# Kernel optimization log

Measured on AMD Instinct MI355X. Metric: run time of the kernel, lower is better.

Reference implementation:

```python
import jax, jax.numpy as jnp
import numpy as np


def conv3d(x, w, b, pad):
    # x: (B,C,D,H,W), w: (O,I,kd,kh,kw)
    y = jax.lax.conv_general_dilated(
        x, w, window_strides=(1, 1, 1), padding=[(pad, pad)] * 3,
        dimension_numbers=('NCDHW', 'OIDHW', 'NCDHW'))
    return y + b[None, :, None, None, None]


def setup_inputs() -> dict:
    key = jax.random.key(0)
    ks = jax.random.split(key, 8)
    B, C, D, H, W = 8, 128, 16, 32, 32
    C8 = C // 8
    return {
        'x': jax.random.normal(ks[0], (B, C, D, H, W), dtype=jnp.float32),
        'gamma': jax.random.normal(ks[1], (1,), dtype=jnp.float32),
        'w_k': jax.random.normal(ks[2], (C8, C, 1, 1, 1), dtype=jnp.float32) * 0.05,
        'b_k': jax.random.normal(ks[3], (C8,), dtype=jnp.float32) * 0.05,
        'w_q': jax.random.normal(ks[4], (C8, C, 1, 1, 1), dtype=jnp.float32) * 0.05,
        'b_q': jax.random.normal(ks[5], (C8,), dtype=jnp.float32) * 0.05,
        'w_v': jax.random.normal(ks[6], (C, C, 3, 3, 3), dtype=jnp.float32) * 0.02,
        'b_v': jax.random.normal(ks[7], (C,), dtype=jnp.float32) * 0.05,
    }


def reference(x, gamma, w_k, b_k, w_q, b_q, w_v, b_v):
    B, C, D, H, W = x.shape
    HW = H * W
    k = conv3d(x, w_k, b_k, 0)   # (B, C/8, D, H, W)
    q = conv3d(x, w_q, b_q, 0)   # (B, C/8, D, H, W)
    v = conv3d(x, w_v, b_v, 1)   # (B, C, D, H, W)

    # --- spatial (P) attention over HW positions, feature dim (C/8)*D ---
    kf = k.reshape(B, -1, HW)
    qf = q.reshape(B, -1, HW)
    # cor[b,s,t] = sum_f k[b,f,s] q[b,f,t]; softmax over t
    A_p = jax.nn.softmax(jnp.einsum('bfs,bft->bst', kf, qf), axis=-1)  # (B,HW,HW)
    vf = v.reshape(B, C * D, HW)
    # Patt[b,m,j] = sum_t v[b,m,t] A_p[b,j,t]  (v @ A_p^T)
    Patt = jnp.einsum('bmt,bjt->bmj', vf, A_p).reshape(B, C, D, H, W)

    # --- depth (D) attention over D slices, feature dim (C/8)*H*W ---
    kd = k.transpose(0, 2, 1, 3, 4).reshape(B, D, -1)
    qd = q.transpose(0, 2, 1, 3, 4).reshape(B, D, -1)
    A_d = jax.nn.softmax(jnp.einsum('bdf,bef->bde', kd, qd), axis=-1)  # (B,D,D)
    vd = v.transpose(0, 2, 1, 3, 4).reshape(B, D, -1)  # (B, D, C*H*W)
    # Datt[b,j,f] = sum_d A_d[b,j,d] vd[b,d,f]
    Datt = jnp.einsum('bjd,bdf->bjf', A_d, vd).reshape(B, D, C, H, W)
    Datt = Datt.transpose(0, 2, 1, 3, 4)  # (B,C,D,H,W)

    return gamma[0] * (Patt + Datt) + x
```

## Files before the change

kernel.cpp:

```cpp
#include <hip/hip_runtime.h>

#define HW   1024
#define DHW  16384

typedef __attribute__((ext_vector_type(8))) short short8;
typedef __attribute__((ext_vector_type(4))) float f32x4;

static __device__ __forceinline__ ushort f2bf(float f) {
  unsigned u = __float_as_uint(f);
  unsigned r = (u + 0x7fffu + ((u >> 16) & 1u)) >> 16;
  return (ushort)r;
}
static __device__ __forceinline__ float bf2f(ushort u) {
  return __uint_as_float(((unsigned)u) << 16);
}
static __device__ __forceinline__ void async_copy16(const ushort* g, ushort* l) {
  __builtin_amdgcn_global_load_lds(
      (const __attribute__((address_space(1))) unsigned int*)g,
      (__attribute__((address_space(3))) unsigned int*)l, 16, 0, 0);
}

__global__ __launch_bounds__(256) void prep_kernel(
    const float* __restrict__ x, const float* __restrict__ wk,
    const float* __restrict__ bk, const float* __restrict__ wq,
    const float* __restrict__ bq, const float* __restrict__ wv,
    float* __restrict__ k, float* __restrict__ q,
    ushort* __restrict__ xt, ushort* __restrict__ wt,
    ushort* __restrict__ zbuf) {
  __shared__ float wks[2048];
  __shared__ float wqs[2048];
  int gid = blockIdx.x;
  int tid = threadIdx.x;
  if (gid >= 512) {
    if (gid == 512 && tid < 512) zbuf[tid] = 0;
    int i = (gid - 512) * 256 + tid;
    int c8 = i & 7;
    int t = i >> 3;
    int o = t & 127; t >>= 7;
    int tap = t % 9; t /= 9;
    int chunk = t & 15;
    int kd = t >> 4;
    wt[i] = f2bf(wv[(size_t)(o * 128 + chunk * 8 + c8) * 27 + kd * 9 + tap]);
    return;
  }
  for (int i = tid; i < 2048; i += 256) {
    int c = i >> 4, o = i & 15;
    wks[i] = wk[o * 128 + c];
    wqs[i] = wq[o * 128 + c];
  }
  __syncthreads();
  int b = gid >> 6, bx = gid & 63;
  int p = bx * 256 + tid;
  int z = p >> 10, hw = p & 1023;
  float ak[16], aq[16];
#pragma unroll
  for (int o = 0; o < 16; ++o) { ak[o] = 0.f; aq[o] = 0.f; }
  const float* xb = x + (size_t)b * 128 * DHW + p;
  ushort* xtp = xt + (((size_t)(b * 16 + z) * 16) * 1024 + hw) * 8;
  for (int chunk = 0; chunk < 16; ++chunk) {
    ushort pack[8];
#pragma unroll
    for (int c8 = 0; c8 < 8; ++c8) {
      int c = chunk * 8 + c8;
      float xv = xb[(size_t)c * DHW];
      pack[c8] = f2bf(xv);
      const float4* wkc = (const float4*)&wks[c * 16];
      const float4* wqc = (const float4*)&wqs[c * 16];
#pragma unroll
      for (int g = 0; g < 4; ++g) {
        float4 wa = wkc[g], wb = wqc[g];
        ak[g * 4 + 0] += wa.x * xv; ak[g * 4 + 1] += wa.y * xv;
        ak[g * 4 + 2] += wa.z * xv; ak[g * 4 + 3] += wa.w * xv;
        aq[g * 4 + 0] += wb.x * xv; aq[g * 4 + 1] += wb.y * xv;
        aq[g * 4 + 2] += wb.z * xv; aq[g * 4 + 3] += wb.w * xv;
      }
    }
    *(uint4*)&xtp[(size_t)chunk * 1024 * 8] = *(const uint4*)pack;
  }
#pragma unroll
  for (int o = 0; o < 16; ++o) {
    k[((size_t)b * 16 + o) * DHW + p] = ak[o] + bk[o];
    q[((size_t)b * 16 + o) * DHW + p] = aq[o] + bq[o];
  }
}

__global__ __launch_bounds__(256, 2) void vconv_mfma_kernel(
    const ushort* __restrict__ xt, const ushort* __restrict__ wt,
    const float* __restrict__ bv, const ushort* __restrict__ zbuf,
    ushort* __restrict__ v) {
  __shared__ __align__(16) ushort xs[1536 * 8];
  __shared__ __align__(16) ushort wsm[2304 * 8];
  int tid = threadIdx.x;
  int wave = tid >> 6;
  int ml = tid & 15;
  int quad = (tid >> 4) & 3;
  int bz = blockIdx.x;
  int b = bz & 7, z = bz >> 3;
  int h0 = blockIdx.y * 8;
  int o0 = blockIdx.z * 64;

  f32x4 acc[4][4];
#pragma unroll
  for (int s = 0; s < 4; ++s)
#pragma unroll
    for (int t = 0; t < 4; ++t) acc[s][t] = (f32x4){0.f, 0.f, 0.f, 0.f};

  int cb0[4];
#pragma unroll
  for (int t = 0; t < 4; ++t)
    cb0[t] = (wave * 2 + (t >> 1)) * 34 + (t & 1) * 16 + ml;

  int xoff[6]; bool okx[6];
#pragma unroll
  for (int it = 0; it < 6; ++it) {
    int i = it * 256 + tid;
    int cu = i / 340;
    int cell = i - cu * 340;
    int hr = cell / 34;
    int wc = cell - hr * 34;
    int h = h0 + hr - 1, ww = wc - 1;
    okx[it] = (i < 1360) && ((unsigned)h < 32u) && ((unsigned)ww < 32u);
    xoff[it] = cu * 1024 + h * 32 + ww;
  }
  int woff[9];
#pragma unroll
  for (int it = 0; it < 9; ++it) {
    int i = it * 256 + tid;
    int cu = i / 576;
    int r = i - cu * 576;
    int tap = r >> 6, ol = r & 63;
    woff[it] = (cu * 9 + tap) * 128 + o0 + ol;
  }

  const int KH[9] = {0, 0, 0, 1, 1, 1, 2, 2, 2};
  const int KW[9] = {0, 1, 2, 0, 1, 2, 0, 1, 2};

  for (int kd = 0; kd < 3; ++kd) {
    int zd = z + kd - 1;
    bool zok = (zd >= 0 && zd < 16);
    int zdc = zok ? zd : 0;
    const ushort* xbase = xt + (size_t)(b * 16 + zdc) * 16 * 1024 * 8;
    for (int cb = 0; cb < 4; ++cb) {
      const ushort* xsb = xbase + (size_t)cb * 4 * 1024 * 8;
      const ushort* wsb = wt + (size_t)(kd * 16 + cb * 4) * 9 * 128 * 8;
#pragma unroll
      for (int it = 0; it < 6; ++it) {
        const ushort* g = (zok && okx[it]) ? xsb + (size_t)xoff[it] * 8 : zbuf;
        async_copy16(g, &xs[(it * 256 + tid) * 8]);
      }
#pragma unroll
      for (int it = 0; it < 9; ++it)
        async_copy16(wsb + (size_t)woff[it] * 8, &wsm[(it * 256 + tid) * 8]);
      __syncthreads();
#pragma unroll
      for (int tap = 0; tap < 9; ++tap) {
        const int kh = KH[tap], kw = KW[tap];
        short8 af[4], bfr[4];
#pragma unroll
        for (int s = 0; s < 4; ++s)
          af[s] = *(const short8*)&wsm[(quad * 576 + tap * 64 + s * 16 + ml) * 8];
#pragma unroll
        for (int t = 0; t < 4; ++t) {
          int cell = cb0[t] + kh * 34 + kw;
          bfr[t] = *(const short8*)&xs[(quad * 340 + cell) * 8];
        }
#pragma unroll
        for (int s = 0; s < 4; ++s)
#pragma unroll
          for (int t = 0; t < 4; ++t)
            acc[s][t] = __builtin_amdgcn_mfma_f32_16x16x32_bf16(af[s], bfr[t], acc[s][t], 0, 0, 0);
      }
      __syncthreads();
    }
  }
#pragma unroll
  for (int s = 0; s < 4; ++s) {
    int o = o0 + s * 16 + quad * 4;
#pragma unroll
    for (int t = 0; t < 4; ++t) {
      int pl = wave * 64 + t * 16 + ml;
      ushort* dst = &v[((size_t)(b * 128 + o) * 16 + z) * 1024 + h0 * 32 + pl];
#pragma unroll
      for (int r = 0; r < 4; ++r)
        dst[(size_t)r * 16384] = f2bf(acc[s][t][r] + bv[o + r]);
    }
  }
}

__global__ __launch_bounds__(256) void kqt_kernel(
    const float* __restrict__ k, const float* __restrict__ q,
    ushort* __restrict__ kT, ushort* __restrict__ qT,
    float* __restrict__ rsum, float* __restrict__ Sd) {
  __shared__ __align__(16) ushort tile[32 * 264];
  int tid = threadIdx.x;
  int t0 = blockIdx.x;
  int b = blockIdx.y;
  if (t0 == 0) {
    *(float4*)&rsum[b * 1024 + tid * 4] = (float4){0.f, 0.f, 0.f, 0.f};
    Sd[b * 256 + tid] = 0.f;
  }
  int h0 = t0 * 32;

  {
    const float* s = k + (size_t)b * 16 * DHW;
    for (int it = 0; it < 32; ++it) {
      int i = it * 256 + tid;
      int oo = i >> 9, zz = (i >> 5) & 15, hl = i & 31;
      tile[hl * 264 + oo * 16 + zz] =
          f2bf(s[(size_t)oo * DHW + zz * 1024 + h0 + hl]);
    }
    __syncthreads();
    ushort* d = kT + ((size_t)b * 1024 + h0) * 256;
    for (int jt = 0; jt < 4; ++jt) {
      int j = jt * 256 + tid;
      int hl = j >> 5, c8 = (j & 31) * 8;
      *(uint4*)&d[(size_t)hl * 256 + c8] = *(const uint4*)&tile[hl * 264 + c8];
    }
    __syncthreads();
  }
  {
    const float* s = q + (size_t)b * 16 * DHW;
    for (int it = 0; it < 32; ++it) {
      int i = it * 256 + tid;
      int oo = i >> 9, zz = (i >> 5) & 15, hl = i & 31;
      tile[hl * 264 + oo * 16 + zz] =
          f2bf(s[(size_t)oo * DHW + zz * 1024 + h0 + hl]);
    }
    __syncthreads();
    ushort* d = qT + ((size_t)b * 1024 + h0) * 256;
    for (int jt = 0; jt < 4; ++jt) {
      int j = jt * 256 + tid;
      int hl = j >> 5, c8 = (j & 31) * 8;
      *(uint4*)&d[(size_t)hl * 256 + c8] = *(const uint4*)&tile[hl * 264 + c8];
    }
  }
}

__global__ __launch_bounds__(256, 2) void att_kernel(
    const ushort* __restrict__ kT, const ushort* __restrict__ qT,
    ushort* __restrict__ A_p, float* __restrict__ rsum,
    const float* __restrict__ k, const float* __restrict__ q,
    float* __restrict__ Sd) {
  __shared__ __align__(16) ushort smem[32768];
  int tid = threadIdx.x;
  int b = blockIdx.x;
  int by = blockIdx.y;

  if (by >= 64) {
    int t = by - 64;
    int dj = t & 15, split = t >> 4;
    float acc[16];
#pragma unroll
    for (int e = 0; e < 16; ++e) acc[e] = 0.f;
    const float* kb = k + (size_t)b * 256 * HW;
    const float* qb = q + (size_t)b * 256 * HW;
    int fend = (split + 1) * 4096;
    for (int f = split * 4096 + tid; f < fend; f += 256) {
      int oc = f >> 10, hw = f & 1023;
      float kv = kb[(oc * 16 + dj) * HW + hw];
#pragma unroll
      for (int e = 0; e < 16; ++e)
        acc[e] += kv * qb[(oc * 16 + e) * HW + hw];
    }
    int lane = tid & 63;
#pragma unroll
    for (int e = 0; e < 16; ++e) {
      float s = acc[e];
      for (int off = 32; off >= 1; off >>= 1) s += __shfl_xor(s, off);
      if (lane == 0) atomicAdd(&Sd[b * 256 + dj * 16 + e], s);
    }
    return;
  }

  int wave = tid >> 6, lane = tid & 63;
  int ml = lane & 15, quad = lane >> 4;
  int wm = wave >> 1, wj = wave & 1;
  int tile = by;
  int m0 = (tile >> 3) * 128;
  int j0 = (tile & 7) * 128;

  f32x4 acc[4][4];
#pragma unroll
  for (int s = 0; s < 4; ++s)
#pragma unroll
    for (int t = 0; t < 4; ++t) acc[s][t] = (f32x4){0.f, 0.f, 0.f, 0.f};

  const ushort* va = kT + ((size_t)b * 1024 + m0) * 256;
  const ushort* pa = qT + ((size_t)b * 1024 + j0) * 256;

  int srow[4], skc[4];
#pragma unroll
  for (int n = 0; n < 4; ++n) {
    int slot = wave * 256 + n * 64 + lane;
    srow[n] = slot >> 3;
    skc[n] = (slot & 7) ^ (srow[n] & 7);
  }

#pragma unroll
  for (int n = 0; n < 4; ++n) {
    async_copy16(va + (size_t)srow[n] * 256 + skc[n] * 8,
                 &smem[(wave * 256 + n * 64) * 8]);
    async_copy16(pa + (size_t)srow[n] * 256 + skc[n] * 8,
                 &smem[8192 + (wave * 256 + n * 64) * 8]);
  }
  __syncthreads();

  for (int t = 0; t < 4; ++t) {
    int cur = (t & 1) * 16384;
    int nxt = 16384 - cur;
    if (t < 3) {
      int kk = (t + 1) * 64;
#pragma unroll
      for (int n = 0; n < 4; ++n) {
        async_copy16(va + (size_t)srow[n] * 256 + kk + skc[n] * 8,
                     &smem[nxt + (wave * 256 + n * 64) * 8]);
        async_copy16(pa + (size_t)srow[n] * 256 + kk + skc[n] * 8,
                     &smem[nxt + 8192 + (wave * 256 + n * 64) * 8]);
      }
    }
#pragma unroll
    for (int ks = 0; ks < 2; ++ks) {
      short8 af[4], bfr[4];
#pragma unroll
      for (int s = 0; s < 4; ++s) {
        int row = wm * 64 + s * 16 + ml;
        int c = ks * 4 + quad;
        af[s] = *(const short8*)&smem[cur + (row * 8 + (c ^ (row & 7))) * 8];
      }
#pragma unroll
      for (int t2 = 0; t2 < 4; ++t2) {
        int row = wj * 64 + t2 * 16 + ml;
        int c = ks * 4 + quad;
        bfr[t2] = *(const short8*)&smem[cur + 8192 + (row * 8 + (c ^ (row & 7))) * 8];
      }
#pragma unroll
      for (int s = 0; s < 4; ++s)
#pragma unroll
        for (int t2 = 0; t2 < 4; ++t2)
          acc[s][t2] = __builtin_amdgcn_mfma_f32_16x16x32_bf16(af[s], bfr[t2], acc[s][t2], 0, 0, 0);
    }
    __syncthreads();
  }

#pragma unroll
  for (int s = 0; s < 4; ++s)
#pragma unroll
    for (int r = 0; r < 4; ++r) {
      float sum = 0.f;
#pragma unroll
      for (int t2 = 0; t2 < 4; ++t2) {
        float p = __expf(acc[s][t2][r]);
        acc[s][t2][r] = p;
        sum += p;
      }
      sum += __shfl_xor(sum, 1);
      sum += __shfl_xor(sum, 2);
      sum += __shfl_xor(sum, 4);
      sum += __shfl_xor(sum, 8);
      if (ml == 0) {
        int m = m0 + wm * 64 + s * 16 + quad * 4 + r;
        atomicAdd(&rsum[b * 1024 + m], sum);
      }
    }
#pragma unroll
  for (int s = 0; s < 4; ++s)
#pragma unroll
    for (int t2 = 0; t2 < 4; ++t2) {
      int j = j0 + wj * 64 + t2 * 16 + ml;
#pragma unroll
      for (int r = 0; r < 4; ++r) {
        int m = m0 + wm * 64 + s * 16 + quad * 4 + r;
        A_p[((size_t)b * 1024 + m) * 1024 + j] = f2bf(acc[s][t2][r]);
      }
    }
}

__global__ __launch_bounds__(256, 2) void combine_mfma_kernel(
    const ushort* __restrict__ vb, const ushort* __restrict__ apb,
    const float* __restrict__ Sd, const float* __restrict__ rsum,
    const float* __restrict__ x, const float* __restrict__ gamma,
    float* __restrict__ out) {
  __shared__ __align__(16) ushort smem[32768];
  __shared__ float Sdl[256];
  __shared__ float Adt[272];
  int tid = threadIdx.x;
  int wave = tid >> 6, lane = tid & 63;
  int ml = lane & 15, quad = lane >> 4;
  int wm = wave >> 1, wj = wave & 1;
  int b = blockIdx.x;
  int tile = blockIdx.y;
  int m0 = (tile >> 3) * 128;
  int j0 = (tile & 7) * 128;
  Sdl[tid] = Sd[b * 256 + tid];

  f32x4 acc[4][4];
#pragma unroll
  for (int s = 0; s < 4; ++s)
#pragma unroll
    for (int t = 0; t < 4; ++t) acc[s][t] = (f32x4){0.f, 0.f, 0.f, 0.f};

  const ushort* va = vb + ((size_t)b * 2048 + m0) * 1024;
  const ushort* pa = apb + ((size_t)b * 1024 + j0) * 1024;

  int srow[4], skc[4];
#pragma unroll
  for (int n = 0; n < 4; ++n) {
    int slot = wave * 256 + n * 64 + lane;
    srow[n] = slot >> 3;
    skc[n] = (slot & 7) ^ (srow[n] & 7);
  }

#pragma unroll
  for (int n = 0; n < 4; ++n) {
    async_copy16(va + (size_t)srow[n] * 1024 + skc[n] * 8,
                 &smem[(wave * 256 + n * 64) * 8]);
    async_copy16(pa + (size_t)srow[n] * 1024 + skc[n] * 8,
                 &smem[8192 + (wave * 256 + n * 64) * 8]);
  }
  __syncthreads();

  if (tid < 16) {
    float m = Sdl[tid * 16];
#pragma unroll
    for (int e = 1; e < 16; ++e) m = fmaxf(m, Sdl[tid * 16 + e]);
    float p[16], s = 0.f;
#pragma unroll
    for (int e = 0; e < 16; ++e) { p[e] = __expf(Sdl[tid * 16 + e] - m); s += p[e]; }
    float inv = 1.f / s;
#pragma unroll
    for (int e = 0; e < 16; ++e) Adt[e * 17 + tid] = p[e] * inv;
  }

  for (int t = 0; t < 16; ++t) {
    int cur = (t & 1) * 16384;
    int nxt = 16384 - cur;
    if (t < 15) {
      int kk = (t + 1) * 64;
#pragma unroll
      for (int n = 0; n < 4; ++n) {
        async_copy16(va + (size_t)srow[n] * 1024 + kk + skc[n] * 8,
                     &smem[nxt + (wave * 256 + n * 64) * 8]);
        async_copy16(pa + (size_t)srow[n] * 1024 + kk + skc[n] * 8,
                     &smem[nxt + 8192 + (wave * 256 + n * 64) * 8]);
      }
    }
#pragma unroll
    for (int ks = 0; ks < 2; ++ks) {
      short8 af[4], bfr[4];
#pragma unroll
      for (int s = 0; s < 4; ++s) {
        int row = wm * 64 + s * 16 + ml;
        int c = ks * 4 + quad;
        af[s] = *(const short8*)&smem[cur + (row * 8 + (c ^ (row & 7))) * 8];
      }
#pragma unroll
      for (int t2 = 0; t2 < 4; ++t2) {
        int row = wj * 64 + t2 * 16 + ml;
        int c = ks * 4 + quad;
        bfr[t2] = *(const short8*)&smem[cur + 8192 + (row * 8 + (c ^ (row & 7))) * 8];
      }
#pragma unroll
      for (int s = 0; s < 4; ++s)
#pragma unroll
        for (int t2 = 0; t2 < 4; ++t2)
          acc[s][t2] = __builtin_amdgcn_mfma_f32_16x16x32_bf16(af[s], bfr[t2], acc[s][t2], 0, 0, 0);
    }
    __syncthreads();
  }

  float invr[4];
#pragma unroll
  for (int t2 = 0; t2 < 4; ++t2)
    invr[t2] = 1.f / rsum[b * 1024 + j0 + wj * 64 + t2 * 16 + ml];
#pragma unroll
  for (int s = 0; s < 4; ++s)
#pragma unroll
    for (int t2 = 0; t2 < 4; ++t2)
#pragma unroll
      for (int r = 0; r < 4; ++r) acc[s][t2][r] *= invr[t2];

  for (int i = tid; i < 2048; i += 256) {
    int row = i >> 4, jc = i & 15;
    uint4 val = *(const uint4*)&vb[((size_t)b * 2048 + m0 + row) * 1024 + j0 + jc * 8];
    *(uint4*)&smem[row * 136 + jc * 8] = val;
  }
  __syncthreads();

#pragma unroll
  for (int d = 0; d < 16; ++d) {
    float ar[4];
#pragma unroll
    for (int r = 0; r < 4; ++r) ar[r] = Adt[d * 17 + quad * 4 + r];
#pragma unroll
    for (int s = 0; s < 4; ++s) {
      const ushort* vrow = &smem[(wm * 64 + s * 16 + d) * 136];
#pragma unroll
      for (int t2 = 0; t2 < 4; ++t2) {
        float vv = bf2f(vrow[wj * 64 + t2 * 16 + ml]);
#pragma unroll
        for (int r = 0; r < 4; ++r) acc[s][t2][r] += ar[r] * vv;
      }
    }
  }

  float g = gamma[0];
#pragma unroll
  for (int s = 0; s < 4; ++s) {
#pragma unroll
    for (int t2 = 0; t2 < 4; ++t2) {
      int jrel = wj * 64 + t2 * 16 + ml;
#pragma unroll
      for (int r = 0; r < 4; ++r) {
        int m = m0 + wm * 64 + s * 16 + quad * 4 + r;
        size_t idx = ((size_t)b * 2048 + m) * 1024 + j0 + jrel;
        out[idx] = g * acc[s][t2][r] + x[idx];
      }
    }
  }
}

extern "C" void kernel_launch(void* const* d_in, const int* in_sizes, int n_in,
                              void* d_out, int out_size, void* d_ws, size_t ws_size,
                              hipStream_t stream) {
  const float* x     = (const float*)d_in[0];
  const float* gamma = (const float*)d_in[1];
  const float* w_k   = (const float*)d_in[2];
  const float* b_k   = (const float*)d_in[3];
  const float* w_q   = (const float*)d_in[4];
  const float* b_q   = (const float*)d_in[5];
  const float* w_v   = (const float*)d_in[6];
  const float* b_v   = (const float*)d_in[7];
  float* out = (float*)d_out;

  float* k    = (float*)d_ws;
  float* q    = k + 2097152;
  float* A_d  = q + 2097152;
  ushort* vbf = (ushort*)(A_d + 2048);
  ushort* apb = vbf + 16777216;
  ushort* wt  = apb + 8388608;
  ushort* zbuf = wt + 442368;
  ushort* xt  = zbuf + 512;
  ushort* kT16 = xt;
  ushort* qT16 = xt + 2097152;
  float* rsum  = (float*)(xt + 4194304);
  float* Sd    = rsum + 8192;

  prep_kernel<<<dim3(2240), 256, 0, stream>>>(x, w_k, b_k, w_q, b_q, w_v,
                                              k, q, xt, wt, zbuf);
  vconv_mfma_kernel<<<dim3(128, 4, 2), 256, 0, stream>>>(xt, wt, b_v, zbuf, vbf);
  kqt_kernel<<<dim3(32, 8), 256, 0, stream>>>(k, q, kT16, qT16, rsum, Sd);
  att_kernel<<<dim3(8, 128), 256, 0, stream>>>(kT16, qT16, apb, rsum, k, q, Sd);
  combine_mfma_kernel<<<dim3(8, 128), 256, 0, stream>>>(vbf, apb, Sd, rsum, x, gamma, out);
}
```

Measured before the change: 333.2 us.

## Fuse k/q bf16 transpose into prep kernel and replace rsum atomics with partials

The prep kernel now writes transposed bf16 kT/qT directly, which removes the separate kqt_kernel launch and its re-read of the fp32 k/q. Row sums from att_kernel are written as 16 per-tile partials instead of atomically added, and combine sums those partials. Buffers are reused: the partials go into the wt region after vconv has finished with it, and kT/qT go into the output buffer before combine overwrites it. The prep kernel's k/q stores become strided 16-byte writes per position, and the correctness of the aliasing depends on kernel ordering.

```diff
diff --git a/kernel.cpp b/kernel.cpp
--- a/kernel.cpp
+++ b/kernel.cpp
@@ -26,12 +26,17 @@
     const float* __restrict__ bq, const float* __restrict__ wv,
     float* __restrict__ k, float* __restrict__ q,
     ushort* __restrict__ xt, ushort* __restrict__ wt,
-    ushort* __restrict__ zbuf) {
+    ushort* __restrict__ zbuf, float* __restrict__ Sd,
+    ushort* __restrict__ kT, ushort* __restrict__ qT) {
   __shared__ float wks[2048];
   __shared__ float wqs[2048];
   int gid = blockIdx.x;
   int tid = threadIdx.x;
   if (gid >= 512) {
+    if (gid == 2240) {
+      for (int i = tid; i < 2048; i += 256) Sd[i] = 0.f;
+      return;
+    }
     if (gid == 512 && tid < 512) zbuf[tid] = 0;
     int i = (gid - 512) * 256 + tid;
     int c8 = i & 7;
@@ -77,11 +82,21 @@
     }
     *(uint4*)&xtp[(size_t)chunk * 1024 * 8] = *(const uint4*)pack;
   }
+  ushort pk[16], pq[16];
 #pragma unroll
   for (int o = 0; o < 16; ++o) {
-    k[((size_t)b * 16 + o) * DHW + p] = ak[o] + bk[o];
-    q[((size_t)b * 16 + o) * DHW + p] = aq[o] + bq[o];
-  }
+    float kv = ak[o] + bk[o];
+    float qv = aq[o] + bq[o];
+    k[((size_t)b * 16 + o) * DHW + p] = kv;
+    q[((size_t)b * 16 + o) * DHW + p] = qv;
+    pk[o] = f2bf(kv);
+    pq[o] = f2bf(qv);
+  }
+  size_t tbase = ((size_t)(b * 1024 + hw)) * 256 + z * 16;
+  *(uint4*)&kT[tbase]     = *(const uint4*)&pk[0];
+  *(uint4*)&kT[tbase + 8] = *(const uint4*)&pk[8];
+  *(uint4*)&qT[tbase]     = *(const uint4*)&pq[0];
+  *(uint4*)&qT[tbase + 8] = *(const uint4*)&pq[8];
 }
 
 __global__ __launch_bounds__(256, 2) void vconv_mfma_kernel(
@@ -187,58 +202,9 @@
   }
 }
 
-__global__ __launch_bounds__(256) void kqt_kernel(
-    const float* __restrict__ k, const float* __restrict__ q,
-    ushort* __restrict__ kT, ushort* __restrict__ qT,
-    float* __restrict__ rsum, float* __restrict__ Sd) {
-  __shared__ __align__(16) ushort tile[32 * 264];
-  int tid = threadIdx.x;
-  int t0 = blockIdx.x;
-  int b = blockIdx.y;
-  if (t0 == 0) {
-    *(float4*)&rsum[b * 1024 + tid * 4] = (float4){0.f, 0.f, 0.f, 0.f};
-    Sd[b * 256 + tid] = 0.f;
-  }
-  int h0 = t0 * 32;
-
-  {
-    const float* s = k + (size_t)b * 16 * DHW;
-    for (int it = 0; it < 32; ++it) {
-      int i = it * 256 + tid;
-      int oo = i >> 9, zz = (i >> 5) & 15, hl = i & 31;
-      tile[hl * 264 + oo * 16 + zz] =
-          f2bf(s[(size_t)oo * DHW + zz * 1024 + h0 + hl]);
-    }
-    __syncthreads();
-    ushort* d = kT + ((size_t)b * 1024 + h0) * 256;
-    for (int jt = 0; jt < 4; ++jt) {
-      int j = jt * 256 + tid;
-      int hl = j >> 5, c8 = (j & 31) * 8;
-      *(uint4*)&d[(size_t)hl * 256 + c8] = *(const uint4*)&tile[hl * 264 + c8];
-    }
-    __syncthreads();
-  }
-  {
-    const float* s = q + (size_t)b * 16 * DHW;
-    for (int it = 0; it < 32; ++it) {
-      int i = it * 256 + tid;
-      int oo = i >> 9, zz = (i >> 5) & 15, hl = i & 31;
-      tile[hl * 264 + oo * 16 + zz] =
-          f2bf(s[(size_t)oo * DHW + zz * 1024 + h0 + hl]);
-    }
-    __syncthreads();
-    ushort* d = qT + ((size_t)b * 1024 + h0) * 256;
-    for (int jt = 0; jt < 4; ++jt) {
-      int j = jt * 256 + tid;
-      int hl = j >> 5, c8 = (j & 31) * 8;
-      *(uint4*)&d[(size_t)hl * 256 + c8] = *(const uint4*)&tile[hl * 264 + c8];
-    }
-  }
-}
-
 __global__ __launch_bounds__(256, 2) void att_kernel(
     const ushort* __restrict__ kT, const ushort* __restrict__ qT,
-    ushort* __restrict__ A_p, float* __restrict__ rsum,
+    ushort* __restrict__ A_p, float* __restrict__ rsum_p,
     const float* __restrict__ k, const float* __restrict__ q,
     float* __restrict__ Sd) {
   __shared__ __align__(16) ushort smem[32768];
@@ -359,7 +325,7 @@
       sum += __shfl_xor(sum, 8);
       if (ml == 0) {
         int m = m0 + wm * 64 + s * 16 + quad * 4 + r;
-        atomicAdd(&rsum[b * 1024 + m], sum);
+        rsum_p[((size_t)(b * 1024 + m)) * 16 + ((tile & 7) << 1) + wj] = sum;
       }
     }
 #pragma unroll
@@ -377,7 +343,7 @@
 
 __global__ __launch_bounds__(256, 2) void combine_mfma_kernel(
     const ushort* __restrict__ vb, const ushort* __restrict__ apb,
-    const float* __restrict__ Sd, const float* __restrict__ rsum,
+    const float* __restrict__ Sd, const float* __restrict__ rsum_p,
     const float* __restrict__ x, const float* __restrict__ gamma,
     float* __restrict__ out) {
   __shared__ __align__(16) ushort smem[32768];
@@ -470,8 +436,14 @@
 
   float invr[4];
 #pragma unroll
-  for (int t2 = 0; t2 < 4; ++t2)
-    invr[t2] = 1.f / rsum[b * 1024 + j0 + wj * 64 + t2 * 16 + ml];
+  for (int t2 = 0; t2 < 4; ++t2) {
+    int j = j0 + wj * 64 + t2 * 16 + ml;
+    const float* pp = &rsum_p[((size_t)(b * 1024 + j)) * 16];
+    float rs = 0.f;
+#pragma unroll
+    for (int p16 = 0; p16 < 16; ++p16) rs += pp[p16];
+    invr[t2] = 1.f / rs;
+  }
 #pragma unroll
   for (int s = 0; s < 4; ++s)
 #pragma unroll
@@ -534,21 +506,20 @@
 
   float* k    = (float*)d_ws;
   float* q    = k + 2097152;
-  float* A_d  = q + 2097152;
-  ushort* vbf = (ushort*)(A_d + 2048);
+  float* Sd   = q + 2097152;
+  ushort* vbf = (ushort*)(Sd + 2048);
   ushort* apb = vbf + 16777216;
   ushort* wt  = apb + 8388608;
   ushort* zbuf = wt + 442368;
   ushort* xt  = zbuf + 512;
-  ushort* kT16 = xt;
-  ushort* qT16 = xt + 2097152;
-  float* rsum  = (float*)(xt + 4194304);
-  float* Sd    = rsum + 8192;
-
-  prep_kernel<<<dim3(2240), 256, 0, stream>>>(x, w_k, b_k, w_q, b_q, w_v,
-                                              k, q, xt, wt, zbuf);
+  float* rsum_p = (float*)wt;
+  ushort* kT16 = (ushort*)out;
+  ushort* qT16 = kT16 + 2097152;
+
+  prep_kernel<<<dim3(2241), 256, 0, stream>>>(x, w_k, b_k, w_q, b_q, w_v,
+                                              k, q, xt, wt, zbuf, Sd,
+                                              kT16, qT16);
   vconv_mfma_kernel<<<dim3(128, 4, 2), 256, 0, stream>>>(xt, wt, b_v, zbuf, vbf);
-  kqt_kernel<<<dim3(32, 8), 256, 0, stream>>>(k, q, kT16, qT16, rsum, Sd);
-  att_kernel<<<dim3(8, 128), 256, 0, stream>>>(kT16, qT16, apb, rsum, k, q, Sd);
-  combine_mfma_kernel<<<dim3(8, 128), 256, 0, stream>>>(vbf, apb, Sd, rsum, x, gamma, out);
-}
+  att_kernel<<<dim3(8, 128), 256, 0, stream>>>(kT16, qT16, apb, rsum_p, k, q, Sd);
+  combine_mfma_kernel<<<dim3(8, 128), 256, 0, stream>>>(vbf, apb, Sd, rsum_p, x, gamma, out);
+}
```

After: 335.4 us. Within noise of the previous version (+0.7%).
